# Performance work log

Hardware: AMD Instinct MI355X
Metric: run time of the kernel (lower is better)

## Reference

```python
import jax, jax.numpy as jnp
import numpy as np

B, S, H = 2, 2048, 2048
NH, NKV, HD = 16, 4, 128          # query heads, kv heads, head_dim
THETA = 10000.0


def setup_inputs() -> dict:
    key = jax.random.key(0)
    ks = jax.random.split(key, 9)
    s = 0.02
    return {
        "hidden_states": jax.random.normal(ks[0], (B, S, H), jnp.float32),
        "q_w": jax.random.normal(ks[1], (NH * HD, H), jnp.float32) * s,
        "q_b": jax.random.normal(ks[2], (NH * HD,), jnp.float32) * s,
        "k_w": jax.random.normal(ks[3], (NKV * HD, H), jnp.float32) * s,
        "k_b": jax.random.normal(ks[4], (NKV * HD,), jnp.float32) * s,
        "v_w": jax.random.normal(ks[5], (NKV * HD, H), jnp.float32) * s,
        "v_b": jax.random.normal(ks[6], (NKV * HD,), jnp.float32) * s,
        "o_w": jax.random.normal(ks[7], (H, NH * HD), jnp.float32) * s,
        "o_b": jax.random.normal(ks[8], (H,), jnp.float32) * s,
    }


def _rotate_half(x):
    x1, x2 = jnp.split(x, 2, axis=-1)
    return jnp.concatenate([-x2, x1], axis=-1)


def reference(hidden_states, q_w, q_b, k_w, k_b, v_w, v_b, o_w, o_b):
    b, s, h = hidden_states.shape
    # QKV projections -> (b, heads, s, hd)
    q = (hidden_states @ q_w.T + q_b).reshape(b, s, NH, HD).transpose(0, 2, 1, 3)
    k = (hidden_states @ k_w.T + k_b).reshape(b, s, NKV, HD).transpose(0, 2, 1, 3)
    v = (hidden_states @ v_w.T + v_b).reshape(b, s, NKV, HD).transpose(0, 2, 1, 3)
    # rotary embedding (default position_ids = arange(s))
    pos = jnp.arange(s, dtype=jnp.float32)
    inv_freq = 1.0 / (THETA ** (jnp.arange(0, HD, 2, dtype=jnp.float32) / HD))
    freqs = pos[:, None] * inv_freq[None, :]          # (s, hd/2)
    emb = jnp.concatenate([freqs, freqs], axis=-1)    # (s, hd)
    cos = jnp.cos(emb)[None, None]                    # (1,1,s,hd)
    sin = jnp.sin(emb)[None, None]
    q = q * cos + _rotate_half(q) * sin
    k = k * cos + _rotate_half(k) * sin
    # GQA: repeat kv heads (repeat_interleave along head dim)
    n_rep = NH // NKV
    k = jnp.repeat(k, n_rep, axis=1)
    v = jnp.repeat(v, n_rep, axis=1)
    # attention (mathematically what the chunked online-softmax intends)
    scores = jnp.einsum('bhqd,bhkd->bhqk', q, k) / np.sqrt(HD).astype(np.float32)
    m = jnp.max(scores, axis=-1, keepdims=True)
    e = jnp.exp(scores - m)
    attn = jnp.einsum('bhqk,bhkd->bhqd', e, v) / (jnp.sum(e, axis=-1, keepdims=True) + 1e-10)
    attn = attn.transpose(0, 2, 1, 3).reshape(b, s, NH * HD)
    return attn @ o_w.T + o_b
```

## Files before the change

kernel.cpp:

```cpp
#include <hip/hip_runtime.h>
#include <hip/hip_bf16.h>
#include <math.h>

typedef __attribute__((ext_vector_type(8))) short bf16x8;
typedef __attribute__((ext_vector_type(4))) float f32x4;
typedef __attribute__((ext_vector_type(16))) float f32x16;
typedef __attribute__((ext_vector_type(4))) unsigned int u32x4;

#if __has_builtin(__builtin_amdgcn_exp2f)
#define EXP2(x) __builtin_amdgcn_exp2f(x)
#else
#define EXP2(x) __expf((x) * 0.6931471805599453f)
#endif

__device__ __forceinline__ ushort f2bf(float f) {
  unsigned u = __float_as_uint(f);
  u = u + 0x7FFFu + ((u >> 16) & 1u);
  return (ushort)(u >> 16);
}
__device__ __forceinline__ float bf2f(ushort h) {
  return __uint_as_float(((unsigned)h) << 16);
}
__device__ __forceinline__ unsigned cvtpk(float a, float b) {
  unsigned r;
  asm("v_cvt_pk_bf16_f32 %0, %1, %2" : "=v"(r) : "v"(a), "v"(b));
  return r;
}
__device__ __forceinline__ void gload_lds16(const ushort* g, ushort* l) {
  __builtin_amdgcn_global_load_lds((const __attribute__((address_space(1))) void*)g,
                                   (__attribute__((address_space(3))) void*)l, 16, 0, 0);
}

__global__ __launch_bounds__(256) void prep_kernel(
    const float* __restrict__ hs, const float* __restrict__ qw,
    const float* __restrict__ kw, const float* __restrict__ vw,
    const float* __restrict__ ow, const float* __restrict__ qb,
    const float* __restrict__ kb, const float* __restrict__ vb,
    ushort* __restrict__ hs_b, ushort* __restrict__ qkvw_b,
    ushort* __restrict__ ow_b, float* __restrict__ qkvb,
    float2* __restrict__ rope_tab)
{
  const int idx = blockIdx.x * 256 + threadIdx.x;
  const int stride = gridDim.x * 256;
  const float4* hs4 = (const float4*)hs;
  const float4* qw4 = (const float4*)qw;
  const float4* kw4 = (const float4*)kw;
  const float4* vw4 = (const float4*)vw;
  const float4* ow4 = (const float4*)ow;
  ushort4* hsb4 = (ushort4*)hs_b;
  ushort4* qkvwb4 = (ushort4*)qkvw_b;
  ushort4* owb4 = (ushort4*)ow_b;

  for (int i = idx; i < 2097152; i += stride) {
    float4 v = hs4[i];
    ushort4 o; o.x=f2bf(v.x); o.y=f2bf(v.y); o.z=f2bf(v.z); o.w=f2bf(v.w);
    hsb4[i] = o;
  }
  for (int i = idx; i < 1048576; i += stride) {
    float4 v = qw4[i];
    ushort4 o; o.x=f2bf(v.x); o.y=f2bf(v.y); o.z=f2bf(v.z); o.w=f2bf(v.w);
    qkvwb4[i] = o;
  }
  for (int i = idx; i < 262144; i += stride) {
    float4 v = kw4[i];
    ushort4 o; o.x=f2bf(v.x); o.y=f2bf(v.y); o.z=f2bf(v.z); o.w=f2bf(v.w);
    qkvwb4[1048576 + i] = o;
  }
  for (int i = idx; i < 262144; i += stride) {
    float4 v = vw4[i];
    ushort4 o; o.x=f2bf(v.x); o.y=f2bf(v.y); o.z=f2bf(v.z); o.w=f2bf(v.w);
    qkvwb4[1310720 + i] = o;
  }
  for (int i = idx; i < 1048576; i += stride) {
    float4 v = ow4[i];
    ushort4 o; o.x=f2bf(v.x); o.y=f2bf(v.y); o.z=f2bf(v.z); o.w=f2bf(v.w);
    owb4[i] = o;
  }
  for (int i = idx; i < 3072; i += stride)
    qkvb[i] = (i < 2048) ? qb[i] : (i < 2560 ? kb[i - 2048] : vb[i - 2560]);
  for (int i = idx; i < 131072; i += stride) {
    int pos = i >> 6, d = i & 63;
    float inv = __expf((float)d * -0.14391156831212787f);
    float ang = (float)pos * inv;
    rope_tab[i] = make_float2(cosf(ang), sinf(ang));
  }
}

__global__ __launch_bounds__(256) void gemm_qkv(
    const ushort* __restrict__ A, const ushort* __restrict__ Bw,
    const float* __restrict__ bias, ushort* __restrict__ qkbuf,
    ushort* __restrict__ vt, const float2* __restrict__ tab)
{
  __shared__ ushort As[128 * 32];
  __shared__ ushort Bs[128 * 32];
  const int t = threadIdx.x;
  const int wv = t >> 6;
  const int lane = t & 63;
  const int qd = lane >> 4, ln = lane & 15;
  const int hwid = blockIdx.x + 32 * blockIdx.y;
  const int logical = (hwid & 7) * 96 + (hwid >> 3);
  const long row0 = (long)(logical & 31) * 128;
  const long col0 = (long)(logical >> 5) * 128;

  f32x4 acc[2][8];
#pragma unroll
  for (int i = 0; i < 2; i++)
#pragma unroll
    for (int j = 0; j < 8; j++) acc[i][j] = (f32x4){0.f, 0.f, 0.f, 0.f};

  const ushort* gA = A + (row0 + (t >> 2)) * 2048l + (t & 3) * 8;
  const ushort* gB = Bw + (col0 + (t >> 2)) * 2048l + (t & 3) * 8;
  ushort* lA = &As[wv * 512];
  ushort* lB = &Bs[wv * 512];
  const long K64 = 64l * 2048;

  for (int kt = 0; kt < 2048; kt += 32) {
    __syncthreads();
    gload_lds16(gA + kt,        lA);
    gload_lds16(gA + kt + K64,  lA + 2048);
    gload_lds16(gB + kt,        lB);
    gload_lds16(gB + kt + K64,  lB + 2048);
    __syncthreads();
    bf16x8 af[2], bf[8];
#pragma unroll
    for (int mi = 0; mi < 2; mi++)
      af[mi] = *(const bf16x8*)&As[(wv * 32 + mi * 16 + ln) * 32 + qd * 8];
#pragma unroll
    for (int ni = 0; ni < 8; ni++)
      bf[ni] = *(const bf16x8*)&Bs[(ni * 16 + ln) * 32 + qd * 8];
#pragma unroll
    for (int mi = 0; mi < 2; mi++)
#pragma unroll
      for (int ni = 0; ni < 8; ni++)
        acc[mi][ni] = __builtin_amdgcn_mfma_f32_16x16x32_bf16(af[mi], bf[ni], acc[mi][ni], 0, 0, 0);
  }

  float bv[8];
#pragma unroll
  for (int ni = 0; ni < 8; ni++) bv[ni] = bias[col0 + ni * 16 + ln];

  if (col0 >= 2560) {
#pragma unroll
    for (int mi = 0; mi < 2; mi++)
#pragma unroll
      for (int ni = 0; ni < 8; ni++)
#pragma unroll
        for (int r = 0; r < 4; r++) {
          long row = row0 + wv * 32 + mi * 16 + qd * 4 + r;
          long col = col0 + ni * 16 + ln - 2560;
          vt[col * 4096 + row] = f2bf(acc[mi][ni][r] + bv[ni]);
        }
  } else {
    const float sc = (col0 < 2048) ? 0.12751744399764505f : 1.0f;
#pragma unroll
    for (int mi = 0; mi < 2; mi++)
#pragma unroll
      for (int ni = 0; ni < 4; ni++) {
        const int d = ni * 16 + ln;
#pragma unroll
        for (int r = 0; r < 4; r++) {
          long row = row0 + wv * 32 + mi * 16 + qd * 4 + r;
          int pos = (int)(row & 2047);
          float2 cs = tab[pos * 64 + d];
          float c = cs.x * sc, s = cs.y * sc;
          float v0 = acc[mi][ni][r]     + bv[ni];
          float v1 = acc[mi][ni + 4][r] + bv[ni + 4];
          ushort* p = qkbuf + row * 2560 + col0 + d;
          p[0]  = f2bf(v0 * c - v1 * s);
          p[64] = f2bf(v1 * c + v0 * s);
        }
      }
  }
}

__global__ __launch_bounds__(256) void gemm_bt(
    const ushort* __restrict__ A, const ushort* __restrict__ Bw,
    const float* __restrict__ bias, float* __restrict__ Cout,
    int K, int ldc)
{
  __shared__ ushort As[128 * 32];
  __shared__ ushort Bs[128 * 32];
  const int t = threadIdx.x;
  const int wv = t >> 6;
  const int lane = t & 63;
  const int qd = lane >> 4, ln = lane & 15;
  const int nwg = gridDim.x * gridDim.y;
  const int cpx = nwg >> 3;
  const int hwid = blockIdx.x + gridDim.x * blockIdx.y;
  const int logical = (hwid & 7) * cpx + (hwid >> 3);
  const long row0 = (long)(logical % gridDim.x) * 128;
  const long col0 = (long)(logical / gridDim.x) * 128;
  const int wm = (wv >> 1) * 64, wn = (wv & 1) * 64;

  f32x4 acc[4][4];
#pragma unroll
  for (int i = 0; i < 4; i++)
#pragma unroll
    for (int j = 0; j < 4; j++) acc[i][j] = (f32x4){0.f, 0.f, 0.f, 0.f};

  const ushort* gA = A + (row0 + (t >> 2)) * (long)K + (t & 3) * 8;
  const ushort* gB = Bw + (col0 + (t >> 2)) * (long)K + (t & 3) * 8;
  ushort* lA = &As[wv * 512];
  ushort* lB = &Bs[wv * 512];
  const long K64 = 64l * K;

  for (int kt = 0; kt < K; kt += 32) {
    __syncthreads();
    gload_lds16(gA + kt,        lA);
    gload_lds16(gA + kt + K64,  lA + 2048);
    gload_lds16(gB + kt,        lB);
    gload_lds16(gB + kt + K64,  lB + 2048);
    __syncthreads();
    bf16x8 af[4], bf[4];
#pragma unroll
    for (int mi = 0; mi < 4; mi++)
      af[mi] = *(const bf16x8*)&As[(wm + mi * 16 + ln) * 32 + qd * 8];
#pragma unroll
    for (int ni = 0; ni < 4; ni++)
      bf[ni] = *(const bf16x8*)&Bs[(wn + ni * 16 + ln) * 32 + qd * 8];
#pragma unroll
    for (int mi = 0; mi < 4; mi++)
#pragma unroll
      for (int ni = 0; ni < 4; ni++)
        acc[mi][ni] = __builtin_amdgcn_mfma_f32_16x16x32_bf16(af[mi], bf[ni], acc[mi][ni], 0, 0, 0);
  }

  float bv[4];
#pragma unroll
  for (int ni = 0; ni < 4; ni++) bv[ni] = bias[col0 + wn + ni * 16 + ln];

#pragma unroll
  for (int mi = 0; mi < 4; mi++)
#pragma unroll
    for (int ni = 0; ni < 4; ni++)
#pragma unroll
      for (int r = 0; r < 4; r++) {
        long row = row0 + wm + mi * 16 + qd * 4 + r;
        long col = col0 + wn + ni * 16 + ln;
        Cout[row * ldc + col] = acc[mi][ni][r] + bv[ni];
      }
}

__global__ __launch_bounds__(256, 2) void flash_kernel(
    const ushort* __restrict__ qk, const ushort* __restrict__ vt,
    ushort* __restrict__ ctx)
{
  __shared__ ushort smem[32768];
  const int t = threadIdx.x, lane = t & 63, wv = t >> 6;
  const int h2 = lane >> 5, m = lane & 31;
  const int hwid = blockIdx.x + 16 * blockIdx.y;
  const int logical = (hwid & 7) * 64 + (hwid >> 3);
  const int bx = logical & 15, by = logical >> 4;
  const int q0 = bx * 128;
  const int b = by >> 4, h = by & 15;
  const long rb = (long)b * 2048;
  const ushort* Qg  = qk + (rb + q0) * 2560 + h * 128;
  const ushort* Kg  = qk + rb * 2560 + 2048 + (h >> 2) * 128;
  const ushort* Vtg = vt + ((long)(h >> 2) * 128) * 4096 + rb;

  bf16x8 qf[8];
  {
    const ushort* qrow = Qg + (long)(wv * 32 + m) * 2560 + h2 * 8;
#pragma unroll
    for (int s2 = 0; s2 < 8; s2++)
      qf[s2] = *(const bf16x8*)(qrow + s2 * 16);
  }

  f32x16 oacc[4];
#pragma unroll
  for (int d = 0; d < 4; d++)
#pragma unroll
    for (int r = 0; r < 16; r++) oacc[d][r] = 0.f;
  float l_run = 0.f;

  const ushort* gK[4];
  const ushort* gV[4];
#pragma unroll
  for (int s = 0; s < 4; s++) {
    int krow = wv * 16 + s * 4 + (lane >> 4);
    int kcd  = (lane & 15) ^ (krow & 15);
    gK[s] = Kg + (long)krow * 2560 + kcd * 8;
    int vrow = wv * 32 + s * 8 + (lane >> 3);
    int vcd  = (lane & 7) ^ ((lane >> 3) & 7);
    gV[s] = Vtg + (long)vrow * 4096 + vcd * 8;
  }
  const int ldsK = wv * 16 * 128;
  const int ldsV = 8192 + wv * 32 * 64;

#pragma unroll
  for (int s = 0; s < 4; s++) gload_lds16(gK[s], smem + ldsK + s * 512);
#pragma unroll
  for (int s = 0; s < 4; s++) gload_lds16(gV[s], smem + ldsV + s * 512);
#pragma unroll
  for (int s = 0; s < 4; s++) { gK[s] += 64l * 2560; gV[s] += 64; }

  const int mk = (m & 15);
  const int mv = (m & 7);

  for (int kt = 0; kt < 2048; kt += 64) {
    const int cb = (kt >> 6) & 1;
    __syncthreads();
    if (kt < 1984) {
      ushort* nb = smem + (cb ^ 1) * 16384;
#pragma unroll
      for (int s = 0; s < 4; s++) gload_lds16(gK[s], nb + ldsK + s * 512);
#pragma unroll
      for (int s = 0; s < 4; s++) gload_lds16(gV[s], nb + ldsV + s * 512);
#pragma unroll
      for (int s = 0; s < 4; s++) { gK[s] += 64l * 2560; gV[s] += 64; }
    }
    const ushort* KsB  = smem + cb * 16384;
    const ushort* VtsB = KsB + 8192;

    float s_sum = 0.f;
#pragma unroll
    for (int kb = 0; kb < 2; kb++) {
      f32x16 sacc;
#pragma unroll
      for (int r = 0; r < 16; r++) sacc[r] = 0.f;
      __builtin_amdgcn_s_setprio(1);
#pragma unroll
      for (int s2 = 0; s2 < 8; s2++) {
        bf16x8 kf = *(const bf16x8*)&KsB[(32 * kb + m) * 128 + ((s2 * 2 + h2) ^ mk) * 8];
        sacc = __builtin_amdgcn_mfma_f32_32x32x16_bf16(kf, qf[s2], sacc, 0, 0, 0);
      }
      __builtin_amdgcn_s_setprio(0);
#pragma unroll
      for (int sh = 0; sh < 2; sh++) {
        float e0 = EXP2(sacc[8 * sh + 0]);
        float e1 = EXP2(sacc[8 * sh + 1]);
        float e2 = EXP2(sacc[8 * sh + 2]);
        float e3 = EXP2(sacc[8 * sh + 3]);
        float e4 = EXP2(sacc[8 * sh + 4]);
        float e5 = EXP2(sacc[8 * sh + 5]);
        float e6 = EXP2(sacc[8 * sh + 6]);
        float e7 = EXP2(sacc[8 * sh + 7]);
        s_sum += ((e0 + e1) + (e2 + e3)) + ((e4 + e5) + (e6 + e7));
        unsigned u0 = cvtpk(e0, e1);
        unsigned u1 = cvtpk(e2, e3);
        unsigned u2 = cvtpk(e4, e5);
        unsigned u3 = cvtpk(e6, e7);
        auto r0 = __builtin_amdgcn_permlane32_swap(u0, u2, false, false);
        auto r1 = __builtin_amdgcn_permlane32_swap(u1, u3, false, false);
        u32x4 pu;
        pu.x = r0[0];
        pu.y = r1[0];
        pu.z = r0[1];
        pu.w = r1[1];
        bf16x8 pfv = __builtin_bit_cast(bf16x8, pu);
        const int s = 2 * kb + sh;
        __builtin_amdgcn_s_setprio(1);
#pragma unroll
        for (int db = 0; db < 4; db++) {
          bf16x8 vf = *(const bf16x8*)&VtsB[(db * 32 + m) * 64 + ((s * 2 + h2) ^ mv) * 8];
          oacc[db] = __builtin_amdgcn_mfma_f32_32x32x16_bf16(vf, pfv, oacc[db], 0, 0, 0);
        }
        __builtin_amdgcn_s_setprio(0);
      }
    }
    l_run += s_sum + __int_as_float(__shfl_xor(__float_as_int(s_sum), 32, 64));
  }

  const float linv = 1.f / (l_run + 1e-10f);
  __syncthreads();
  ushort* Obuf = smem;
#pragma unroll
  for (int db = 0; db < 4; db++)
#pragma unroll
    for (int r = 0; r < 16; r++) {
      int d = db * 32 + (r & 3) + 8 * (r >> 2) + 4 * h2;
      Obuf[(wv * 32 + m) * 136 + d] = f2bf(oacc[db][r] * linv);
    }
  __syncthreads();
  {
    int qr = t >> 1;
    ushort* dst = ctx + (rb + q0 + qr) * 2048 + h * 128;
#pragma unroll
    for (int c = 0; c < 8; c++) {
      int off = ((t & 1) * 8 + c) * 8;
      *(uint4*)(dst + off) = *(const uint4*)&Obuf[qr * 136 + off];
    }
  }
}

extern "C" void kernel_launch(void* const* d_in, const int* in_sizes, int n_in,
                              void* d_out, int out_size, void* d_ws, size_t ws_size,
                              hipStream_t stream)
{
  const float* hs = (const float*)d_in[0];
  const float* qw = (const float*)d_in[1];
  const float* qb = (const float*)d_in[2];
  const float* kw = (const float*)d_in[3];
  const float* kb = (const float*)d_in[4];
  const float* vw = (const float*)d_in[5];
  const float* vb = (const float*)d_in[6];
  const float* ow = (const float*)d_in[7];
  const float* ob = (const float*)d_in[8];

  char* ws = (char*)d_ws;
  ushort* hs_b   = (ushort*)(ws);
  ushort* qkvw_b = (ushort*)(ws + 16777216);
  ushort* ow_b   = (ushort*)(ws + 29360128);
  float*  qkvb   = (float*) (ws + 37748736);
  ushort* qkbuf  = (ushort*)(ws + 37761024);
  ushort* vtbuf  = (ushort*)(ws + 58732544);
  ushort* ctx    = (ushort*)(ws + 62926848);
  float2* rope_tab = (float2*)(ws + 62926848);

  prep_kernel<<<1024, 256, 0, stream>>>(hs, qw, kw, vw, ow, qb, kb, vb,
                                        hs_b, qkvw_b, ow_b, qkvb, rope_tab);
  gemm_qkv<<<dim3(32, 24), 256, 0, stream>>>(hs_b, qkvw_b, qkvb, qkbuf, vtbuf,
                                             rope_tab);
  flash_kernel<<<dim3(16, 32), 256, 0, stream>>>(qkbuf, vtbuf, ctx);
  gemm_bt<<<dim3(32, 16), 256, 0, stream>>>(ctx, ow_b, ob, (float*)d_out,
                                            2048, 2048);
}
```

Before: 343.8 us.

## Double-buffer LDS tiles in GEMMs and drop XCD block remapping

Both GEMM kernels now use two LDS buffers. Each iteration prefetches the next K-slice into the idle buffer while computing on the current one, which removes one of the two barriers per iteration and overlaps global-to-LDS loads with MFMA work. Separately, the XCD-aware block-index swizzle is removed from gemm_qkv, gemm_bt and flash_kernel in favour of plain blockIdx mapping. That could lower L2 locality across XCDs, and the larger LDS footprint may reduce occupancy.

```diff
diff --git a/kernel.cpp b/kernel.cpp
--- a/kernel.cpp
+++ b/kernel.cpp
@@ -91,16 +91,13 @@
     const float* __restrict__ bias, ushort* __restrict__ qkbuf,
     ushort* __restrict__ vt, const float2* __restrict__ tab)
 {
-  __shared__ ushort As[128 * 32];
-  __shared__ ushort Bs[128 * 32];
+  __shared__ ushort sm[2][8192];
   const int t = threadIdx.x;
   const int wv = t >> 6;
   const int lane = t & 63;
   const int qd = lane >> 4, ln = lane & 15;
-  const int hwid = blockIdx.x + 32 * blockIdx.y;
-  const int logical = (hwid & 7) * 96 + (hwid >> 3);
-  const long row0 = (long)(logical & 31) * 128;
-  const long col0 = (long)(logical >> 5) * 128;
+  const long row0 = (long)blockIdx.x * 128;
+  const long col0 = (long)blockIdx.y * 128;
 
   f32x4 acc[2][8];
 #pragma unroll
@@ -110,24 +107,33 @@
 
   const ushort* gA = A + (row0 + (t >> 2)) * 2048l + (t & 3) * 8;
   const ushort* gB = Bw + (col0 + (t >> 2)) * 2048l + (t & 3) * 8;
-  ushort* lA = &As[wv * 512];
-  ushort* lB = &Bs[wv * 512];
+  const int lo = wv * 512;
   const long K64 = 64l * 2048;
 
+  gload_lds16(gA,       &sm[0][lo]);
+  gload_lds16(gA + K64, &sm[0][lo + 2048]);
+  gload_lds16(gB,       &sm[0][4096 + lo]);
+  gload_lds16(gB + K64, &sm[0][4096 + lo + 2048]);
+
   for (int kt = 0; kt < 2048; kt += 32) {
+    const int cb = (kt >> 5) & 1;
     __syncthreads();
-    gload_lds16(gA + kt,        lA);
-    gload_lds16(gA + kt + K64,  lA + 2048);
-    gload_lds16(gB + kt,        lB);
-    gload_lds16(gB + kt + K64,  lB + 2048);
-    __syncthreads();
+    if (kt < 2016) {
+      ushort* nb = &sm[cb ^ 1][0];
+      gload_lds16(gA + kt + 32,       nb + lo);
+      gload_lds16(gA + kt + 32 + K64, nb + lo + 2048);
+      gload_lds16(gB + kt + 32,       nb + 4096 + lo);
+      gload_lds16(gB + kt + 32 + K64, nb + 4096 + lo + 2048);
+    }
+    const ushort* Asb = &sm[cb][0];
+    const ushort* Bsb = &sm[cb][4096];
     bf16x8 af[2], bf[8];
 #pragma unroll
     for (int mi = 0; mi < 2; mi++)
-      af[mi] = *(const bf16x8*)&As[(wv * 32 + mi * 16 + ln) * 32 + qd * 8];
+      af[mi] = *(const bf16x8*)&Asb[(wv * 32 + mi * 16 + ln) * 32 + qd * 8];
 #pragma unroll
     for (int ni = 0; ni < 8; ni++)
-      bf[ni] = *(const bf16x8*)&Bs[(ni * 16 + ln) * 32 + qd * 8];
+      bf[ni] = *(const bf16x8*)&Bsb[(ni * 16 + ln) * 32 + qd * 8];
 #pragma unroll
     for (int mi = 0; mi < 2; mi++)
 #pragma unroll
@@ -178,18 +184,13 @@
     const float* __restrict__ bias, float* __restrict__ Cout,
     int K, int ldc)
 {
-  __shared__ ushort As[128 * 32];
-  __shared__ ushort Bs[128 * 32];
+  __shared__ ushort sm[2][8192];
   const int t = threadIdx.x;
   const int wv = t >> 6;
   const int lane = t & 63;
   const int qd = lane >> 4, ln = lane & 15;
-  const int nwg = gridDim.x * gridDim.y;
-  const int cpx = nwg >> 3;
-  const int hwid = blockIdx.x + gridDim.x * blockIdx.y;
-  const int logical = (hwid & 7) * cpx + (hwid >> 3);
-  const long row0 = (long)(logical % gridDim.x) * 128;
-  const long col0 = (long)(logical / gridDim.x) * 128;
+  const long row0 = (long)blockIdx.x * 128;
+  const long col0 = (long)blockIdx.y * 128;
   const int wm = (wv >> 1) * 64, wn = (wv & 1) * 64;
 
   f32x4 acc[4][4];
@@ -200,24 +201,33 @@
 
   const ushort* gA = A + (row0 + (t >> 2)) * (long)K + (t & 3) * 8;
   const ushort* gB = Bw + (col0 + (t >> 2)) * (long)K + (t & 3) * 8;
-  ushort* lA = &As[wv * 512];
-  ushort* lB = &Bs[wv * 512];
+  const int lo = wv * 512;
   const long K64 = 64l * K;
 
+  gload_lds16(gA,       &sm[0][lo]);
+  gload_lds16(gA + K64, &sm[0][lo + 2048]);
+  gload_lds16(gB,       &sm[0][4096 + lo]);
+  gload_lds16(gB + K64, &sm[0][4096 + lo + 2048]);
+
   for (int kt = 0; kt < K; kt += 32) {
+    const int cb = (kt >> 5) & 1;
     __syncthreads();
-    gload_lds16(gA + kt,        lA);
-    gload_lds16(gA + kt + K64,  lA + 2048);
-    gload_lds16(gB + kt,        lB);
-    gload_lds16(gB + kt + K64,  lB + 2048);
-    __syncthreads();
+    if (kt + 32 < K) {
+      ushort* nb = &sm[cb ^ 1][0];
+      gload_lds16(gA + kt + 32,       nb + lo);
+      gload_lds16(gA + kt + 32 + K64, nb + lo + 2048);
+      gload_lds16(gB + kt + 32,       nb + 4096 + lo);
+      gload_lds16(gB + kt + 32 + K64, nb + 4096 + lo + 2048);
+    }
+    const ushort* Asb = &sm[cb][0];
+    const ushort* Bsb = &sm[cb][4096];
     bf16x8 af[4], bf[4];
 #pragma unroll
     for (int mi = 0; mi < 4; mi++)
-      af[mi] = *(const bf16x8*)&As[(wm + mi * 16 + ln) * 32 + qd * 8];
+      af[mi] = *(const bf16x8*)&Asb[(wm + mi * 16 + ln) * 32 + qd * 8];
 #pragma unroll
     for (int ni = 0; ni < 4; ni++)
-      bf[ni] = *(const bf16x8*)&Bs[(wn + ni * 16 + ln) * 32 + qd * 8];
+      bf[ni] = *(const bf16x8*)&Bsb[(wn + ni * 16 + ln) * 32 + qd * 8];
 #pragma unroll
     for (int mi = 0; mi < 4; mi++)
 #pragma unroll
@@ -248,11 +258,8 @@
   __shared__ ushort smem[32768];
   const int t = threadIdx.x, lane = t & 63, wv = t >> 6;
   const int h2 = lane >> 5, m = lane & 31;
-  const int hwid = blockIdx.x + 16 * blockIdx.y;
-  const int logical = (hwid & 7) * 64 + (hwid >> 3);
-  const int bx = logical & 15, by = logical >> 4;
-  const int q0 = bx * 128;
-  const int b = by >> 4, h = by & 15;
+  const int q0 = blockIdx.x * 128;
+  const int b = blockIdx.y >> 4, h = blockIdx.y & 15;
   const long rb = (long)b * 2048;
   const ushort* Qg  = qk + (rb + q0) * 2560 + h * 128;
   const ushort* Kg  = qk + rb * 2560 + 2048 + (h >> 2) * 128;
```

New measurement: 311.5 us. 1.1x faster.
